# Kernel tuning notes

Measured on AMD Instinct MI355X. Metric: run time of the kernel, lower is better.

## Reference

```python
import jax, jax.numpy as jnp
import numpy as np

BN_EPS = 1e-5

def _haar_details(x):
    # pywt.dwt2(x, 'haar') details for even H, W.
    # Block [[p, q], [r, s]] with p = x[2i,2j], q = x[2i,2j+1], r = x[2i+1,2j], s = x[2i+1,2j+1].
    # cH ('da'): detail along rows, approx along cols; cV ('ad'); cD ('dd').
    B, C, H, W = x.shape
    xb = x.reshape(B, C, H // 2, 2, W // 2, 2)
    p = xb[:, :, :, 0, :, 0]
    q = xb[:, :, :, 0, :, 1]
    r = xb[:, :, :, 1, :, 0]
    s = xb[:, :, :, 1, :, 1]
    cH = (p + q - r - s) * 0.5
    cV = (p - q + r - s) * 0.5
    cD = (p - q - r + s) * 0.5
    return cH, cV, cD

def setup_inputs() -> dict:
    key = jax.random.key(0)
    k1, k2 = jax.random.split(key)
    B, C, H, W = 8, 256, 128, 128
    x = jax.random.normal(k1, (B, C, H, W), dtype=jnp.float32)
    conv_w = jax.random.normal(k2, (C, 4 * C), dtype=jnp.float32) * (1.0 / np.sqrt(4 * C))
    gamma = jnp.ones((C,), dtype=jnp.float32)
    beta = jnp.zeros((C,), dtype=jnp.float32)
    return {"x": x, "conv_w": conv_w, "gamma": gamma, "beta": beta}

def reference(x, conv_w, gamma, beta):
    B, C, H, W = x.shape
    # Original detaches the wavelet branch (CPU numpy path) -> stop_gradient.
    xs = jax.lax.stop_gradient(x)
    cH, cV, cD = _haar_details(xs)
    # Bilinear upsample to (H, W); jax.image.resize bilinear == torch align_corners=False.
    up = lambda t: jax.image.resize(t, (B, C, H, W), method="bilinear")
    enhanced = jnp.concatenate([x, up(cH), up(cV), up(cD)], axis=1)  # [B, 4C, H, W]
    # 1x1 conv, no bias.
    y = jnp.einsum("bchw,oc->bohw", enhanced, conv_w)  # [B, C, H, W]
    # BatchNorm2d, training-mode (batch statistics, biased variance).
    mean = jnp.mean(y, axis=(0, 2, 3), keepdims=True)
    var = jnp.mean((y - mean) ** 2, axis=(0, 2, 3), keepdims=True)
    y_hat = (y - mean) * jax.lax.rsqrt(var + BN_EPS)
    out = jax.nn.relu(y_hat * gamma[None, :, None, None] + beta[None, :, None, None])
    return out
```

## Files before the change

kernel.cpp:

```cpp
#include <hip/hip_runtime.h>
#include <hip/hip_bf16.h>

typedef __bf16 bf16;
typedef __bf16 bf16x4 __attribute__((ext_vector_type(4)));
typedef __bf16 bf16x8 __attribute__((ext_vector_type(8)));
typedef float  f32x4  __attribute__((ext_vector_type(4)));

__global__ __launch_bounds__(256) void prep_w(const float* __restrict__ w,
                                              bf16* __restrict__ wb) {
    const int o = blockIdx.x, c = threadIdx.x;
    const float* wr = w + o * 1024;
    const float w1 = wr[c], w2 = wr[256 + c], w3 = wr[512 + c], w4 = wr[768 + c];
    bf16* wo_ = wb + o * 1280;
    wo_[c]              = (bf16)w1;
    wo_[256 + 0*256 + c] = (bf16)(0.5f * ( w2 + w3 + w4));
    wo_[256 + 1*256 + c] = (bf16)(0.5f * ( w2 - w3 - w4));
    wo_[256 + 2*256 + c] = (bf16)(0.5f * (-w2 + w3 - w4));
    wo_[256 + 3*256 + c] = (bf16)(0.5f * (-w2 - w3 + w4));
}

__device__ __forceinline__ int tix(int row, int chunk, int lo) {
    int g = (row & 7) ^ ((row >> 2) & 7);
    return row * 256 + (((chunk ^ g) << 3) | lo);
}

__global__ __launch_bounds__(512, 4) void fused_x(const float* __restrict__ x,
                                                  const bf16* __restrict__ W,
                                                  bf16* __restrict__ z,
                                                  bf16* __restrict__ y1) {
    __shared__ bf16 tile[128 * 256];
    const int bid = blockIdx.x;
    const int half = bid & 1, j = (bid >> 1) & 63, b = bid >> 7;
    const int t = threadIdx.x;
    const int wave = t >> 6, lane = t & 63;
    const int quad = lane >> 4, l16 = lane & 15;
    const int wo2 = wave * 32;

    #pragma unroll
    for (int it = 0; it < 2; ++it) {
        const int a   = it * 512 + t;
        const int c8  = a >> 5;
        const int rem = a & 31;
        const int dlt = rem >> 4, w4 = rem & 15;
        const float* xp = x + (((size_t)b * 256 + c8 * 8) * 128 + (2*j + dlt)) * 128
                            + half * 64 + w4 * 4;
        float4 v[8];
        #pragma unroll
        for (int i = 0; i < 8; ++i)
            v[i] = *(const float4*)(xp + (size_t)i * 16384);
        #pragma unroll
        for (int e = 0; e < 4; ++e) {
            bf16x8 o8;
            #pragma unroll
            for (int i = 0; i < 8; ++i) o8[i] = (bf16)((&v[i].x)[e]);
            const int pos = dlt * 64 + w4 * 4 + e;
            *(bf16x8*)&tile[tix(pos, c8, 0)] = o8;
        }
    }

    bf16x8 wf_cur[2], wf_nxt[2];
    #pragma unroll
    for (int jj = 0; jj < 2; ++jj)
        wf_cur[jj] = *(const bf16x8*)(W +
            (size_t)(wo2 + jj * 16 + l16) * 1280 + quad * 8);

    __syncthreads();

    {
        f32x4 acc[8][2] = {};
        #pragma unroll
        for (int kk = 0; kk < 256; kk += 32) {
            if (kk < 224) {
                #pragma unroll
                for (int jj = 0; jj < 2; ++jj)
                    wf_nxt[jj] = *(const bf16x8*)(W +
                        (size_t)(wo2 + jj * 16 + l16) * 1280 + kk + 32 + quad * 8);
            } else {
                #pragma unroll
                for (int jj = 0; jj < 2; ++jj)
                    wf_nxt[jj] = *(const bf16x8*)(W +
                        (size_t)(wo2 + jj * 16 + l16) * 1280 + 256 + quad * 8);
            }
            const int kc0 = kk >> 3;
            #pragma unroll
            for (int i2 = 0; i2 < 8; ++i2) {
                const bf16x8 xf = *(const bf16x8*)&tile[tix(i2 * 16 + l16,
                                                            kc0 + quad, 0)];
                #pragma unroll
                for (int jj = 0; jj < 2; ++jj)
                    acc[i2][jj] = __builtin_amdgcn_mfma_f32_16x16x32_bf16(
                        xf, wf_cur[jj], acc[i2][jj], 0, 0, 0);
            }
            #pragma unroll
            for (int jj = 0; jj < 2; ++jj) wf_cur[jj] = wf_nxt[jj];
        }

        #pragma unroll
        for (int jj = 0; jj < 2; ++jj)
            wf_nxt[jj] = *(const bf16x8*)(W +
                (size_t)(wo2 + jj * 16 + l16) * 1280 + 256 + 32 + quad * 8);

        #pragma unroll
        for (int i2 = 0; i2 < 8; ++i2) {
            int p = i2 * 16 + quad * 4;
            int h = 2 * j + (p >> 6), wc = half * 64 + (p & 63);
            #pragma unroll
            for (int jj = 0; jj < 2; ++jj) {
                int o = wo2 + jj * 16 + l16;
                bf16x4 vv;
                #pragma unroll
                for (int r = 0; r < 4; ++r) vv[r] = (bf16)acc[i2][jj][r];
                *(bf16x4*)(y1 + ((size_t)b * 256 + o) * 16384 + h * 128 + wc) = vv;
            }
        }
    }

    f32x4 acc2[2][2] = {};
    #pragma unroll
    for (int kz = 0; kz < 1024; kz += 32) {
        bf16x8 wf_nx2[2];
        if (kz < 960) {
            #pragma unroll
            for (int jj = 0; jj < 2; ++jj)
                wf_nx2[jj] = *(const bf16x8*)(W +
                    (size_t)(wo2 + jj * 16 + l16) * 1280 + 256 + kz + 64 + quad * 8);
        }
        const int tap = kz >> 8;
        const int dlt = tap >> 1, par = tap & 1;
        const int kc0 = (kz & 255) >> 3;
        bf16x8 af[2];
        #pragma unroll
        for (int mi = 0; mi < 2; ++mi)
            af[mi] = *(const bf16x8*)&tile[tix(dlt * 64 + 2 * (mi * 16 + l16) + par,
                                               kc0 + quad, 0)];
        #pragma unroll
        for (int mi = 0; mi < 2; ++mi)
            #pragma unroll
            for (int jj = 0; jj < 2; ++jj)
                acc2[mi][jj] = __builtin_amdgcn_mfma_f32_16x16x32_bf16(
                    af[mi], wf_cur[jj], acc2[mi][jj], 0, 0, 0);
        #pragma unroll
        for (int jj = 0; jj < 2; ++jj) { wf_cur[jj] = wf_nxt[jj]; wf_nxt[jj] = wf_nx2[jj]; }
    }

    #pragma unroll
    for (int mi = 0; mi < 2; ++mi) {
        #pragma unroll
        for (int jj = 0; jj < 2; ++jj) {
            int o = wo2 + jj * 16 + l16;
            int cw = half * 32 + mi * 16 + quad * 4;
            bf16x4 vv;
            #pragma unroll
            for (int r = 0; r < 4; ++r) vv[r] = (bf16)acc2[mi][jj][r];
            *(bf16x4*)(z + ((size_t)b * 256 + o) * 4096 + j * 64 + cw) = vv;
        }
    }
}

#define ZS 68

__device__ __forceinline__ void load_zplane(const bf16* zp, float* zs, int t) {
    #pragma unroll
    for (int i = 0; i < 2; ++i) {
        int idx = (i * 256 + t) * 8;
        int j = idx >> 6, k = idx & 63;
        bf16x8 v = *(const bf16x8*)(zp + idx);
        float4 a, bq;
        a.x  = (float)v[0]; a.y  = (float)v[1]; a.z  = (float)v[2]; a.w  = (float)v[3];
        bq.x = (float)v[4]; bq.y = (float)v[5]; bq.z = (float)v[6]; bq.w = (float)v[7];
        *(float4*)&zs[j * ZS + k]     = a;
        *(float4*)&zs[j * ZS + k + 4] = bq;
    }
}

__device__ __forceinline__ void up8(const float* zs, int base, float* u) {
    int h = base >> 7, w0 = base & 127;
    int j0 = h >> 1;
    int jn = (h & 1) ? min(j0 + 1, 63) : max(j0 - 1, 0);
    int K = w0 >> 1;
    const float* r0 = zs + j0 * ZS;
    const float* r1 = zs + jn * ZS;
    float z0[6], z1[6];
    #pragma unroll
    for (int d = 0; d < 6; ++d) {
        int kc = min(max(K - 1 + d, 0), 63);
        z0[d] = r0[kc];
        z1[d] = r1[kc];
    }
    #pragma unroll
    for (int e = 0; e < 8; ++e) {
        int a = (e >> 1) + 1;
        int bb = (e & 1) ? a + 1 : a - 1;
        u[e] = 0.5625f * z0[a] + 0.1875f * (z0[bb] + z1[a]) + 0.0625f * z1[bb];
    }
}

__global__ __launch_bounds__(256) void stats_k(const bf16* __restrict__ y1,
                                               const bf16* __restrict__ z,
                                               float* __restrict__ stats) {
    __shared__ float zs[64 * ZS];
    __shared__ float red[8];
    const int bid = blockIdx.x;
    const int o = bid & 255, b = bid >> 8;
    const int t = threadIdx.x;
    const bf16* zp = z + ((size_t)b * 256 + o) * 4096;
    const bf16* yp = y1 + ((size_t)b * 256 + o) * 16384;
    load_zplane(zp, zs, t);
    bf16x8 yv[8];
    #pragma unroll
    for (int i = 0; i < 8; ++i)
        yv[i] = *(const bf16x8*)(yp + (i * 256 + t) * 8);
    __syncthreads();
    float s = 0.f, ss = 0.f;
    #pragma unroll
    for (int i = 0; i < 8; ++i) {
        int base = (i * 256 + t) * 8;
        float u[8];
        up8(zs, base, u);
        #pragma unroll
        for (int e = 0; e < 8; ++e) {
            float y = (float)yv[i][e] + u[e];
            s += y; ss += y * y;
        }
    }
    #pragma unroll
    for (int off = 32; off > 0; off >>= 1) {
        s += __shfl_down(s, off);
        ss += __shfl_down(ss, off);
    }
    if ((t & 63) == 0) { red[t >> 6] = s; red[4 + (t >> 6)] = ss; }
    __syncthreads();
    if (t == 0) {
        atomicAdd(&stats[o],       red[0] + red[1] + red[2] + red[3]);
        atomicAdd(&stats[256 + o], red[4] + red[5] + red[6] + red[7]);
    }
}

__global__ __launch_bounds__(256) void apply_k(const bf16* __restrict__ y1,
                                               const bf16* __restrict__ z,
                                               const float* __restrict__ stats,
                                               const float* __restrict__ gamma,
                                               const float* __restrict__ beta,
                                               float* __restrict__ out) {
    __shared__ float zs[64 * ZS];
    const int bid = blockIdx.x;
    const int o = bid & 255, b = bid >> 8;
    const int t = threadIdx.x;
    const bf16* zp = z + ((size_t)b * 256 + o) * 4096;
    const bf16* yp = y1 + ((size_t)b * 256 + o) * 16384;
    float* op = out + ((size_t)b * 256 + o) * 16384;
    const float n = 131072.f;
    float mean = stats[o] / n;
    float var = stats[256 + o] / n - mean * mean;
    float sc = rsqrtf(var + 1e-5f) * gamma[o];
    float sh = beta[o] - mean * sc;
    load_zplane(zp, zs, t);
    bf16x8 yv[8];
    #pragma unroll
    for (int i = 0; i < 8; ++i)
        yv[i] = *(const bf16x8*)(yp + (i * 256 + t) * 8);
    __syncthreads();
    #pragma unroll
    for (int i = 0; i < 8; ++i) {
        int base = (i * 256 + t) * 8;
        float u[8];
        up8(zs, base, u);
        float4 o0, o1;
        o0.x = fmaxf(fmaf((float)yv[i][0] + u[0], sc, sh), 0.f);
        o0.y = fmaxf(fmaf((float)yv[i][1] + u[1], sc, sh), 0.f);
        o0.z = fmaxf(fmaf((float)yv[i][2] + u[2], sc, sh), 0.f);
        o0.w = fmaxf(fmaf((float)yv[i][3] + u[3], sc, sh), 0.f);
        o1.x = fmaxf(fmaf((float)yv[i][4] + u[4], sc, sh), 0.f);
        o1.y = fmaxf(fmaf((float)yv[i][5] + u[5], sc, sh), 0.f);
        o1.z = fmaxf(fmaf((float)yv[i][6] + u[6], sc, sh), 0.f);
        o1.w = fmaxf(fmaf((float)yv[i][7] + u[7], sc, sh), 0.f);
        *(float4*)(op + base) = o0;
        *(float4*)(op + base + 4) = o1;
    }
}

extern "C" void kernel_launch(void* const* d_in, const int* in_sizes, int n_in,
                              void* d_out, int out_size, void* d_ws, size_t ws_size,
                              hipStream_t stream) {
    const float* x      = (const float*)d_in[0];
    const float* conv_w = (const float*)d_in[1];
    const float* gamma  = (const float*)d_in[2];
    const float* beta   = (const float*)d_in[3];
    float* out = (float*)d_out;

    char* ws = (char*)d_ws;
    bf16*  Wbf   = (bf16*)ws;
    bf16*  z     = (bf16*)(ws + (1ll << 20));
    float* stats = (float*)(ws + (17ll << 20));
    bf16*  y1    = (bf16*)(ws + (17ll << 20) + (1ll << 16));

    hipMemsetAsync(stats, 0, 4096, stream);
    prep_w<<<256, 256, 0, stream>>>(conv_w, Wbf);
    fused_x<<<1024, 512, 0, stream>>>(x, Wbf, z, y1);
    stats_k<<<2048, 256, 0, stream>>>(y1, z, stats);
    apply_k<<<2048, 256, 0, stream>>>(y1, z, stats, gamma, beta, out);
}
```

Measured before the change: 347.1 us.

## Separate bilinear upsample into horizontal LDS pass and prefetch MFMA A-fragments

The stats and apply kernels now split the 2D bilinear upsample into a horizontal pass that writes a 64x128 float plane to LDS, followed by a vertical blend read with vectorized float4 loads. This replaces the per-thread scalar 6+6 gathers and 4-term blends. The cost is an extra 33 KB of LDS per block and an extra barrier, which may lower occupancy. Separately, the GEMM's second phase double-buffers the LDS A-fragment loads two steps ahead, matching the existing weight prefetch, to hide LDS latency behind MFMAs.

```diff
diff --git a/kernel.cpp b/kernel.cpp
--- a/kernel.cpp
+++ b/kernel.cpp
@@ -115,32 +115,41 @@
         }
     }
 
+    bf16x8 af_c[2], af_n[2];
+    #pragma unroll
+    for (int mi = 0; mi < 2; ++mi) {
+        af_c[mi] = *(const bf16x8*)&tile[tix(2 * (mi * 16 + l16), quad, 0)];
+        af_n[mi] = *(const bf16x8*)&tile[tix(2 * (mi * 16 + l16), 4 + quad, 0)];
+    }
+
     f32x4 acc2[2][2] = {};
     #pragma unroll
     for (int kz = 0; kz < 1024; kz += 32) {
-        bf16x8 wf_nx2[2];
+        bf16x8 wf_2[2], af_2[2];
         if (kz < 960) {
+            const int kz2 = kz + 64;
             #pragma unroll
             for (int jj = 0; jj < 2; ++jj)
-                wf_nx2[jj] = *(const bf16x8*)(W +
-                    (size_t)(wo2 + jj * 16 + l16) * 1280 + 256 + kz + 64 + quad * 8);
-        }
-        const int tap = kz >> 8;
-        const int dlt = tap >> 1, par = tap & 1;
-        const int kc0 = (kz & 255) >> 3;
-        bf16x8 af[2];
-        #pragma unroll
-        for (int mi = 0; mi < 2; ++mi)
-            af[mi] = *(const bf16x8*)&tile[tix(dlt * 64 + 2 * (mi * 16 + l16) + par,
-                                               kc0 + quad, 0)];
+                wf_2[jj] = *(const bf16x8*)(W +
+                    (size_t)(wo2 + jj * 16 + l16) * 1280 + 256 + kz2 + quad * 8);
+            const int tap2 = kz2 >> 8;
+            const int dlt2 = tap2 >> 1, par2 = tap2 & 1;
+            const int kc2 = (kz2 & 255) >> 3;
+            #pragma unroll
+            for (int mi = 0; mi < 2; ++mi)
+                af_2[mi] = *(const bf16x8*)&tile[tix(
+                    dlt2 * 64 + 2 * (mi * 16 + l16) + par2, kc2 + quad, 0)];
+        }
         #pragma unroll
         for (int mi = 0; mi < 2; ++mi)
             #pragma unroll
             for (int jj = 0; jj < 2; ++jj)
                 acc2[mi][jj] = __builtin_amdgcn_mfma_f32_16x16x32_bf16(
-                    af[mi], wf_cur[jj], acc2[mi][jj], 0, 0, 0);
-        #pragma unroll
-        for (int jj = 0; jj < 2; ++jj) { wf_cur[jj] = wf_nxt[jj]; wf_nxt[jj] = wf_nx2[jj]; }
+                    af_c[mi], wf_cur[jj], acc2[mi][jj], 0, 0, 0);
+        #pragma unroll
+        for (int mi = 0; mi < 2; ++mi) { af_c[mi] = af_n[mi]; af_n[mi] = af_2[mi]; }
+        #pragma unroll
+        for (int jj = 0; jj < 2; ++jj) { wf_cur[jj] = wf_nxt[jj]; wf_nxt[jj] = wf_2[jj]; }
     }
 
     #pragma unroll
@@ -158,6 +167,7 @@
 }
 
 #define ZS 68
+#define HS 132
 
 __device__ __forceinline__ void load_zplane(const bf16* zp, float* zs, int t) {
     #pragma unroll
@@ -173,32 +183,45 @@
     }
 }
 
-__device__ __forceinline__ void up8(const float* zs, int base, float* u) {
-    int h = base >> 7, w0 = base & 127;
-    int j0 = h >> 1;
-    int jn = (h & 1) ? min(j0 + 1, 63) : max(j0 - 1, 0);
-    int K = w0 >> 1;
-    const float* r0 = zs + j0 * ZS;
-    const float* r1 = zs + jn * ZS;
-    float z0[6], z1[6];
-    #pragma unroll
-    for (int d = 0; d < 6; ++d) {
-        int kc = min(max(K - 1 + d, 0), 63);
-        z0[d] = r0[kc];
-        z1[d] = r1[kc];
-    }
-    #pragma unroll
-    for (int e = 0; e < 8; ++e) {
-        int a = (e >> 1) + 1;
-        int bb = (e & 1) ? a + 1 : a - 1;
-        u[e] = 0.5625f * z0[a] + 0.1875f * (z0[bb] + z1[a]) + 0.0625f * z1[bb];
-    }
+__device__ __forceinline__ void hup_pass(const float* zs, float* hup, int t) {
+    const int r = t >> 2, seg = t & 3, k0 = seg * 16;
+    const float* zr = zs + r * ZS;
+    float zz[18];
+    #pragma unroll
+    for (int d = 0; d < 18; ++d)
+        zz[d] = zr[min(max(k0 - 1 + d, 0), 63)];
+    float* hr = hup + r * HS + seg * 32;
+    #pragma unroll
+    for (int i = 0; i < 8; ++i) {
+        float e0 = zz[2 * i + 1], e1 = zz[2 * i + 2];
+        float4 o;
+        o.x = 0.75f * e0 + 0.25f * zz[2 * i];
+        o.y = 0.75f * e0 + 0.25f * e1;
+        o.z = 0.75f * e1 + 0.25f * e0;
+        o.w = 0.75f * e1 + 0.25f * zz[2 * i + 3];
+        *(float4*)&hr[4 * i] = o;
+    }
+}
+
+__device__ __forceinline__ void up8v(const float* hup, int base, float* u) {
+    const int h = base >> 7, w0 = base & 127;
+    const int j0 = h >> 1;
+    const int jn = (h & 1) ? min(j0 + 1, 63) : max(j0 - 1, 0);
+    const float* r0 = hup + j0 * HS + w0;
+    const float* r1 = hup + jn * HS + w0;
+    float4 a0 = *(const float4*)r0, a1 = *(const float4*)(r0 + 4);
+    float4 b0 = *(const float4*)r1, b1 = *(const float4*)(r1 + 4);
+    u[0] = 0.75f * a0.x + 0.25f * b0.x;  u[1] = 0.75f * a0.y + 0.25f * b0.y;
+    u[2] = 0.75f * a0.z + 0.25f * b0.z;  u[3] = 0.75f * a0.w + 0.25f * b0.w;
+    u[4] = 0.75f * a1.x + 0.25f * b1.x;  u[5] = 0.75f * a1.y + 0.25f * b1.y;
+    u[6] = 0.75f * a1.z + 0.25f * b1.z;  u[7] = 0.75f * a1.w + 0.25f * b1.w;
 }
 
 __global__ __launch_bounds__(256) void stats_k(const bf16* __restrict__ y1,
                                                const bf16* __restrict__ z,
                                                float* __restrict__ stats) {
     __shared__ float zs[64 * ZS];
+    __shared__ float hup[64 * HS];
     __shared__ float red[8];
     const int bid = blockIdx.x;
     const int o = bid & 255, b = bid >> 8;
@@ -211,12 +234,14 @@
     for (int i = 0; i < 8; ++i)
         yv[i] = *(const bf16x8*)(yp + (i * 256 + t) * 8);
     __syncthreads();
+    hup_pass(zs, hup, t);
+    __syncthreads();
     float s = 0.f, ss = 0.f;
     #pragma unroll
     for (int i = 0; i < 8; ++i) {
         int base = (i * 256 + t) * 8;
         float u[8];
-        up8(zs, base, u);
+        up8v(hup, base, u);
         #pragma unroll
         for (int e = 0; e < 8; ++e) {
             float y = (float)yv[i][e] + u[e];
@@ -243,6 +268,7 @@
                                                const float* __restrict__ beta,
                                                float* __restrict__ out) {
     __shared__ float zs[64 * ZS];
+    __shared__ float hup[64 * HS];
     const int bid = blockIdx.x;
     const int o = bid & 255, b = bid >> 8;
     const int t = threadIdx.x;
@@ -260,11 +286,13 @@
     for (int i = 0; i < 8; ++i)
         yv[i] = *(const bf16x8*)(yp + (i * 256 + t) * 8);
     __syncthreads();
+    hup_pass(zs, hup, t);
+    __syncthreads();
     #pragma unroll
     for (int i = 0; i < 8; ++i) {
         int base = (i * 256 + t) * 8;
         float u[8];
-        up8(zs, base, u);
+        up8v(hup, base, u);
         float4 o0, o1;
         o0.x = fmaxf(fmaf((float)yv[i][0] + u[0], sc, sh), 0.f);
         o0.y = fmaxf(fmaf((float)yv[i][1] + u[1], sc, sh), 0.f);
```

After: 347.5 us. About the same (+0.1%).

## Split stats/apply planes into row segments and batch-load weights per tap in fused GEMM

Applied to the files above, without the earlier changes.

The stats and apply kernels now process a quarter-plane (32 output rows) per block, loading only the 18 needed z rows (with halo) into a much smaller shared buffer. This quadruples the grid and lowers per-block LDS and register use, aiming for better occupancy and latency hiding. In the fused GEMM kernel, the second-phase weight loads are issued up front as 16 fragments per tap behind a sched_barrier instead of being rotated through a register pipeline. The batched loads raise register pressure, and the smaller blocks cost more atomics and more redundant halo reads.

```diff
diff --git a/kernel.cpp b/kernel.cpp
--- a/kernel.cpp
+++ b/kernel.cpp
@@ -75,11 +75,6 @@
                 for (int jj = 0; jj < 2; ++jj)
                     wf_nxt[jj] = *(const bf16x8*)(W +
                         (size_t)(wo2 + jj * 16 + l16) * 1280 + kk + 32 + quad * 8);
-            } else {
-                #pragma unroll
-                for (int jj = 0; jj < 2; ++jj)
-                    wf_nxt[jj] = *(const bf16x8*)(W +
-                        (size_t)(wo2 + jj * 16 + l16) * 1280 + 256 + quad * 8);
             }
             const int kc0 = kk >> 3;
             #pragma unroll
@@ -91,14 +86,11 @@
                     acc[i2][jj] = __builtin_amdgcn_mfma_f32_16x16x32_bf16(
                         xf, wf_cur[jj], acc[i2][jj], 0, 0, 0);
             }
-            #pragma unroll
-            for (int jj = 0; jj < 2; ++jj) wf_cur[jj] = wf_nxt[jj];
-        }
-
-        #pragma unroll
-        for (int jj = 0; jj < 2; ++jj)
-            wf_nxt[jj] = *(const bf16x8*)(W +
-                (size_t)(wo2 + jj * 16 + l16) * 1280 + 256 + 32 + quad * 8);
+            if (kk < 224) {
+                #pragma unroll
+                for (int jj = 0; jj < 2; ++jj) wf_cur[jj] = wf_nxt[jj];
+            }
+        }
 
         #pragma unroll
         for (int i2 = 0; i2 < 8; ++i2) {
@@ -117,30 +109,29 @@
 
     f32x4 acc2[2][2] = {};
     #pragma unroll
-    for (int kz = 0; kz < 1024; kz += 32) {
-        bf16x8 wf_nx2[2];
-        if (kz < 960) {
-            #pragma unroll
-            for (int jj = 0; jj < 2; ++jj)
-                wf_nx2[jj] = *(const bf16x8*)(W +
-                    (size_t)(wo2 + jj * 16 + l16) * 1280 + 256 + kz + 64 + quad * 8);
-        }
-        const int tap = kz >> 8;
+    for (int tap = 0; tap < 4; ++tap) {
         const int dlt = tap >> 1, par = tap & 1;
-        const int kc0 = (kz & 255) >> 3;
-        bf16x8 af[2];
-        #pragma unroll
-        for (int mi = 0; mi < 2; ++mi)
-            af[mi] = *(const bf16x8*)&tile[tix(dlt * 64 + 2 * (mi * 16 + l16) + par,
-                                               kc0 + quad, 0)];
-        #pragma unroll
-        for (int mi = 0; mi < 2; ++mi)
-            #pragma unroll
-            for (int jj = 0; jj < 2; ++jj)
-                acc2[mi][jj] = __builtin_amdgcn_mfma_f32_16x16x32_bf16(
-                    af[mi], wf_cur[jj], acc2[mi][jj], 0, 0, 0);
-        #pragma unroll
-        for (int jj = 0; jj < 2; ++jj) { wf_cur[jj] = wf_nxt[jj]; wf_nxt[jj] = wf_nx2[jj]; }
+        bf16x8 wfc[16];
+        #pragma unroll
+        for (int s = 0; s < 16; ++s)
+            wfc[s] = *(const bf16x8*)(W +
+                (size_t)(wo2 + (s & 1) * 16 + l16) * 1280 +
+                256 + tap * 256 + (s >> 1) * 32 + quad * 8);
+        __builtin_amdgcn_sched_barrier(0);
+        #pragma unroll
+        for (int ks = 0; ks < 8; ++ks) {
+            bf16x8 af[2];
+            #pragma unroll
+            for (int mi = 0; mi < 2; ++mi)
+                af[mi] = *(const bf16x8*)&tile[tix(
+                    dlt * 64 + 2 * (mi * 16 + l16) + par, ks * 4 + quad, 0)];
+            #pragma unroll
+            for (int mi = 0; mi < 2; ++mi)
+                #pragma unroll
+                for (int jj = 0; jj < 2; ++jj)
+                    acc2[mi][jj] = __builtin_amdgcn_mfma_f32_16x16x32_bf16(
+                        af[mi], wfc[ks * 2 + jj], acc2[mi][jj], 0, 0, 0);
+        }
     }
 
     #pragma unroll
@@ -159,27 +150,14 @@
 
 #define ZS 68
 
-__device__ __forceinline__ void load_zplane(const bf16* zp, float* zs, int t) {
-    #pragma unroll
-    for (int i = 0; i < 2; ++i) {
-        int idx = (i * 256 + t) * 8;
-        int j = idx >> 6, k = idx & 63;
-        bf16x8 v = *(const bf16x8*)(zp + idx);
-        float4 a, bq;
-        a.x  = (float)v[0]; a.y  = (float)v[1]; a.z  = (float)v[2]; a.w  = (float)v[3];
-        bq.x = (float)v[4]; bq.y = (float)v[5]; bq.z = (float)v[6]; bq.w = (float)v[7];
-        *(float4*)&zs[j * ZS + k]     = a;
-        *(float4*)&zs[j * ZS + k + 4] = bq;
-    }
-}
-
-__device__ __forceinline__ void up8(const float* zs, int base, float* u) {
-    int h = base >> 7, w0 = base & 127;
-    int j0 = h >> 1;
-    int jn = (h & 1) ? min(j0 + 1, 63) : max(j0 - 1, 0);
-    int K = w0 >> 1;
-    const float* r0 = zs + j0 * ZS;
-    const float* r1 = zs + jn * ZS;
+__device__ __forceinline__ void up8s(const float* zs, int gbase, int base_j,
+                                     float* u) {
+    const int h = gbase >> 7, w0 = gbase & 127;
+    const int j0 = h >> 1;
+    const int jn = (h & 1) ? min(j0 + 1, 63) : max(j0 - 1, 0);
+    const float* r0 = zs + (j0 - base_j) * ZS;
+    const float* r1 = zs + (jn - base_j) * ZS;
+    const int K = w0 >> 1;
     float z0[6], z1[6];
     #pragma unroll
     for (int d = 0; d < 6; ++d) {
@@ -195,28 +173,42 @@
     }
 }
 
+__device__ __forceinline__ void load_zseg(const bf16* zp, float* zs,
+                                          int base_j, int t) {
+    if (t < 144) {
+        const int r = t >> 3, k8 = t & 7;
+        const int gr = min(max(base_j + r, 0), 63);
+        bf16x8 v = *(const bf16x8*)(zp + gr * 64 + k8 * 8);
+        float4 a, bq;
+        a.x  = (float)v[0]; a.y  = (float)v[1]; a.z  = (float)v[2]; a.w  = (float)v[3];
+        bq.x = (float)v[4]; bq.y = (float)v[5]; bq.z = (float)v[6]; bq.w = (float)v[7];
+        *(float4*)&zs[r * ZS + k8 * 8]     = a;
+        *(float4*)&zs[r * ZS + k8 * 8 + 4] = bq;
+    }
+}
+
 __global__ __launch_bounds__(256) void stats_k(const bf16* __restrict__ y1,
                                                const bf16* __restrict__ z,
                                                float* __restrict__ stats) {
-    __shared__ float zs[64 * ZS];
+    __shared__ float zs[18 * ZS];
     __shared__ float red[8];
     const int bid = blockIdx.x;
-    const int o = bid & 255, b = bid >> 8;
+    const int seg = bid & 3, o = (bid >> 2) & 255, b = bid >> 10;
     const int t = threadIdx.x;
+    const int base_j = seg * 16 - 1;
     const bf16* zp = z + ((size_t)b * 256 + o) * 4096;
-    const bf16* yp = y1 + ((size_t)b * 256 + o) * 16384;
-    load_zplane(zp, zs, t);
-    bf16x8 yv[8];
-    #pragma unroll
-    for (int i = 0; i < 8; ++i)
-        yv[i] = *(const bf16x8*)(yp + (i * 256 + t) * 8);
+    const bf16* yp = y1 + ((size_t)b * 256 + o) * 16384 + seg * 4096;
+    load_zseg(zp, zs, base_j, t);
+    bf16x8 yv[2];
+    yv[0] = *(const bf16x8*)(yp + t * 8);
+    yv[1] = *(const bf16x8*)(yp + 2048 + t * 8);
     __syncthreads();
     float s = 0.f, ss = 0.f;
     #pragma unroll
-    for (int i = 0; i < 8; ++i) {
-        int base = (i * 256 + t) * 8;
+    for (int i = 0; i < 2; ++i) {
+        const int gbase = seg * 4096 + i * 2048 + t * 8;
         float u[8];
-        up8(zs, base, u);
+        up8s(zs, gbase, base_j, u);
         #pragma unroll
         for (int e = 0; e < 8; ++e) {
             float y = (float)yv[i][e] + u[e];
@@ -242,29 +234,30 @@
                                                const float* __restrict__ gamma,
                                                const float* __restrict__ beta,
                                                float* __restrict__ out) {
-    __shared__ float zs[64 * ZS];
+    __shared__ float zs[18 * ZS];
     const int bid = blockIdx.x;
-    const int o = bid & 255, b = bid >> 8;
+    const int seg = bid & 3, o = (bid >> 2) & 255, b = bid >> 10;
     const int t = threadIdx.x;
+    const int base_j = seg * 16 - 1;
     const bf16* zp = z + ((size_t)b * 256 + o) * 4096;
-    const bf16* yp = y1 + ((size_t)b * 256 + o) * 16384;
-    float* op = out + ((size_t)b * 256 + o) * 16384;
+    const bf16* yp = y1 + ((size_t)b * 256 + o) * 16384 + seg * 4096;
+    float* op = out + ((size_t)b * 256 + o) * 16384 + seg * 4096;
     const float n = 131072.f;
     float mean = stats[o] / n;
     float var = stats[256 + o] / n - mean * mean;
     float sc = rsqrtf(var + 1e-5f) * gamma[o];
     float sh = beta[o] - mean * sc;
-    load_zplane(zp, zs, t);
-    bf16x8 yv[8];
-    #pragma unroll
-    for (int i = 0; i < 8; ++i)
-        yv[i] = *(const bf16x8*)(yp + (i * 256 + t) * 8);
-    __syncthreads();
-    #pragma unroll
-    for (int i = 0; i < 8; ++i) {
-        int base = (i * 256 + t) * 8;
+    load_zseg(zp, zs, base_j, t);
+    bf16x8 yv[2];
+    yv[0] = *(const bf16x8*)(yp + t * 8);
+    yv[1] = *(const bf16x8*)(yp + 2048 + t * 8);
+    __syncthreads();
+    #pragma unroll
+    for (int i = 0; i < 2; ++i) {
+        const int lbase = i * 2048 + t * 8;
+        const int gbase = seg * 4096 + lbase;
         float u[8];
-        up8(zs, base, u);
+        up8s(zs, gbase, base_j, u);
         float4 o0, o1;
         o0.x = fmaxf(fmaf((float)yv[i][0] + u[0], sc, sh), 0.f);
         o0.y = fmaxf(fmaf((float)yv[i][1] + u[1], sc, sh), 0.f);
@@ -274,8 +267,8 @@
         o1.y = fmaxf(fmaf((float)yv[i][5] + u[5], sc, sh), 0.f);
         o1.z = fmaxf(fmaf((float)yv[i][6] + u[6], sc, sh), 0.f);
         o1.w = fmaxf(fmaf((float)yv[i][7] + u[7], sc, sh), 0.f);
-        *(float4*)(op + base) = o0;
-        *(float4*)(op + base + 4) = o1;
+        *(float4*)(op + lbase) = o0;
+        *(float4*)(op + lbase + 4) = o1;
     }
 }
 
@@ -297,6 +290,6 @@
     hipMemsetAsync(stats, 0, 4096, stream);
     prep_w<<<256, 256, 0, stream>>>(conv_w, Wbf);
     fused_x<<<1024, 512, 0, stream>>>(x, Wbf, z, y1);
-    stats_k<<<2048, 256, 0, stream>>>(y1, z, stats);
-    apply_k<<<2048, 256, 0, stream>>>(y1, z, stats, gamma, beta, out);
-}
+    stats_k<<<8192, 256, 0, stream>>>(y1, z, stats);
+    apply_k<<<8192, 256, 0, stream>>>(y1, z, stats, gamma, beta, out);
+}
```

Measured after the change: 339.9 us. 2.1% less time.
